# Performance work log

Hardware: AMD Instinct MI355X
Metric: run time of the kernel (lower is better)

The kernel has to match this reference:

```python
import jax, jax.numpy as jnp
import numpy as np

B, S, D = 2, 1024, 768      # batch, seq, d_model
F, F_UP = 8192, 8192        # downstream / upstream dictionary sizes
K = 64                      # top-k of the downstream AE
MASK_DENSITY = 0.05         # fraction of allowed feature-feature connections


def setup_inputs() -> dict:
    key = jax.random.key(0)
    ks = jax.random.split(key, 12)
    inv_sqrt_d = 1.0 / np.sqrt(D)
    resid = jax.random.normal(ks[0], (B, S, D), dtype=jnp.float32)
    # upstream pruned features: k-sparse-ish non-negative activations
    pruned0 = jax.nn.relu(jax.random.normal(ks[1], (B, S, F_UP)) - 2.0).astype(jnp.float32)
    pruned1 = jax.nn.relu(jax.random.normal(ks[2], (B, S, F_UP)) - 2.0).astype(jnp.float32)
    feature_buffer = jnp.zeros((B, S, F), dtype=jnp.float32)
    W_enc = jax.random.normal(ks[3], (F, D), dtype=jnp.float32) * inv_sqrt_d
    b_enc = jax.random.normal(ks[4], (F,), dtype=jnp.float32) * 0.01
    W_dec = jax.random.normal(ks[5], (F, D), dtype=jnp.float32) * inv_sqrt_d
    b_dec = jax.random.normal(ks[6], (D,), dtype=jnp.float32) * 0.01
    W_dec_up0 = jax.random.normal(ks[7], (F_UP, D), dtype=jnp.float32) * inv_sqrt_d
    W_dec_up1 = jax.random.normal(ks[8], (F_UP, D), dtype=jnp.float32) * inv_sqrt_d
    b_dec_up0 = jax.random.normal(ks[9], (D,), dtype=jnp.float32) * 0.01
    b_dec_up1 = jax.random.normal(ks[10], (D,), dtype=jnp.float32) * 0.01
    km0, km1 = jax.random.split(ks[11])
    mask0 = (jax.random.uniform(km0, (F, F_UP)) < MASK_DENSITY).astype(jnp.float32)
    mask1 = (jax.random.uniform(km1, (F, F_UP)) < MASK_DENSITY).astype(jnp.float32)
    return {
        "resid": resid, "pruned0": pruned0, "pruned1": pruned1,
        "feature_buffer": feature_buffer,
        "W_enc": W_enc, "b_enc": b_enc, "W_dec": W_dec, "b_dec": b_dec,
        "W_dec_up0": W_dec_up0, "W_dec_up1": W_dec_up1,
        "b_dec_up0": b_dec_up0, "b_dec_up1": b_dec_up1,
        "mask0": mask0, "mask1": mask1, "k": K,
    }


def reference(resid, pruned0, pruned1, feature_buffer,
              W_enc, b_enc, W_dec, b_dec,
              W_dec_up0, W_dec_up1, b_dec_up0, b_dec_up1,
              mask0, mask1, k):
    # initial contributions: encode the cached residual stream, [B,S,F]
    approx = jnp.einsum("bsd,fd->bsf", resid, W_enc)
    upstream_bias = b_dec_up0 + b_dec_up1
    # accumulate connection-masked upstream contributions
    for pruned, W_dec_up, mask in ((pruned0, W_dec_up0, mask0),
                                   (pruned1, W_dec_up1, mask1)):
        # masked virtual weights: [F, F_up]
        virtual = jnp.einsum("fd,ud->fu", W_enc, W_dec_up) * mask
        approx = approx + jnp.einsum("bsu,fu->bsf", pruned, virtual)
    # bias correction: project summed upstream decoder biases, add encoder bias
    approx = approx + jnp.einsum("fd,d->f", W_enc, upstream_bias) + b_enc
    # topk (unsorted set equals torch's sorted=False), relu, scatter into buffer
    top_vals, top_idx = jax.lax.top_k(approx, k)        # [B,S,k]
    top_vals = jax.nn.relu(top_vals)
    Bn, Sn, Fn = feature_buffer.shape
    bi = jnp.arange(Bn)[:, None, None]
    si = jnp.arange(Sn)[None, :, None]
    feat_buffer = jnp.zeros_like(feature_buffer).at[bi, si, top_idx].set(top_vals)
    # dense decode
    reconstructions = jnp.einsum("bsf,fd->bsd", feat_buffer, W_dec) + b_dec
    return feat_buffer, reconstructions
```

## Files before the change

### kernel.cpp

```cpp
#include <hip/hip_runtime.h>
#include <stdint.h>

typedef unsigned long long u64;
typedef unsigned short u16;

#define F_DIM 8192
#define U_DIM 8192
#define D_DIM 768
#define NTOK  2048
#define KSEL  64
#define ROWCAP 544
#define TILE  256
#define NFT   32
#define NUT   32
#define DCH   32
#define ENTCAP 3840
#define NBIN  1024
#define FT    128
#define TT    128
#define NTT   16
#define PCAP  16

__global__ void k_bias(const float* __restrict__ Wenc, const float* __restrict__ benc,
                       const float* __restrict__ b0, const float* __restrict__ b1,
                       float* __restrict__ t_bias) {
    int wid = threadIdx.x >> 6, lane = threadIdx.x & 63;
    int f = blockIdx.x * 4 + wid;
    const float* row = Wenc + (size_t)f * D_DIM;
    float s = 0.f;
    for (int j = lane; j < D_DIM; j += 64) s += row[j] * (b0[j] + b1[j]);
    #pragma unroll
    for (int off = 32; off; off >>= 1) s += __shfl_down(s, off, 64);
    if (lane == 0) t_bias[f] = s + benc[f];
}

__global__ void k_mask_scan(const float* __restrict__ mask0, const float* __restrict__ mask1,
                            int* __restrict__ rowcnt_tile, u64* __restrict__ bitmap) {
    __shared__ int rc[TILE][4];
    int ut = blockIdx.x, ft = blockIdx.y, l = blockIdx.z;
    const float* mask = l ? mask1 : mask0;
    int tid = threadIdx.x, lane = tid & 63, wid = tid >> 6;
    int u = ut * TILE + tid;
    int f0 = ft * TILE;
    u64* bm = bitmap + (((size_t)(l * NFT + ft) * NUT + ut) * TILE) * 4;
    for (int fl = 0; fl < TILE; ++fl) {
        float v = mask[(size_t)(f0 + fl) * U_DIM + u];
        u64 bal = __ballot(v != 0.0f);
        if (lane == 0) { bm[(size_t)fl * 4 + wid] = bal; rc[fl][wid] = __popcll(bal); }
    }
    __syncthreads();
    rowcnt_tile[(size_t)(l * NUT + ut) * F_DIM + f0 + tid] =
        rc[tid][0] + rc[tid][1] + rc[tid][2] + rc[tid][3];
}

__global__ void k_row_prefix(const int* __restrict__ rowcnt_tile, int* __restrict__ base_r,
                             int* __restrict__ rowcnt_tot) {
    int idx = blockIdx.x * blockDim.x + threadIdx.x;
    int l = idx >> 13, f = idx & (F_DIM - 1);
    int run = 0;
    for (int ut = 0; ut < NUT; ++ut) {
        int c = rowcnt_tile[(size_t)(l * NUT + ut) * F_DIM + f];
        base_r[(size_t)(l * NUT + ut) * F_DIM + f] = run;
        run += c;
    }
    rowcnt_tot[l * F_DIM + f] = run < ROWCAP ? run : ROWCAP;
}

__global__ __launch_bounds__(256, 2) void k_virt_build(
        const float* __restrict__ Wenc, const float* __restrict__ Wup0,
        const float* __restrict__ Wup1, const u64* __restrict__ bitmap,
        const int* __restrict__ base_r, u16* __restrict__ csr_u, float* __restrict__ csr_v) {
    __shared__ u64 bm[TILE][4];
    __shared__ int cs[TILE];
    __shared__ unsigned char entu[ENTCAP];
    __shared__ float acc[ENTCAP];
    __shared__ float wu_t[DCH][TILE + 1];
    int ut = blockIdx.x, ft = blockIdx.y, l = blockIdx.z;
    const float* Wup = l ? Wup1 : Wup0;
    int tid = threadIdx.x;
    int u0 = ut * TILE, f0 = ft * TILE;

    const u64* gbm = bitmap + (((size_t)(l * NFT + ft) * NUT + ut) * TILE) * 4;
    for (int i = tid; i < TILE * 4; i += 256) ((u64*)bm)[i] = gbm[i];
    __syncthreads();

    int cnt = 0;
    #pragma unroll
    for (int w = 0; w < 4; ++w) cnt += (int)__popcll(bm[tid][w]);
    cs[tid] = cnt;
    __syncthreads();
    for (int off = 1; off < 256; off <<= 1) {
        int v = (tid >= off) ? cs[tid - off] : 0;
        __syncthreads();
        cs[tid] += v;
        __syncthreads();
    }
    int cstart = cs[tid] - cnt;
    {
        int i = 0;
        #pragma unroll
        for (int w = 0; w < 4; ++w) {
            u64 word = bm[tid][w];
            while (word) {
                int b = __builtin_ctzll(word); word &= word - 1;
                int p = cstart + i;
                if (p < ENTCAP) entu[p] = (unsigned char)(w * 64 + b);
                ++i;
            }
        }
    }
    for (int i = tid; i < ENTCAP; i += 256) acc[i] = 0.f;
    __syncthreads();

    float we[DCH];
    for (int d0 = 0; d0 < D_DIM; d0 += DCH) {
        const float* ur = Wup + (size_t)(u0 + tid) * D_DIM + d0;
        #pragma unroll
        for (int j = 0; j < DCH; j += 4) {
            float4 t4 = *(const float4*)(ur + j);
            wu_t[j][tid] = t4.x; wu_t[j + 1][tid] = t4.y;
            wu_t[j + 2][tid] = t4.z; wu_t[j + 3][tid] = t4.w;
        }
        const float* wr = Wenc + (size_t)(f0 + tid) * D_DIM + d0;
        #pragma unroll
        for (int j = 0; j < DCH; j += 4) {
            float4 t4 = *(const float4*)(wr + j);
            we[j] = t4.x; we[j + 1] = t4.y; we[j + 2] = t4.z; we[j + 3] = t4.w;
        }
        __syncthreads();
        for (int i = 0; i < cnt; ++i) {
            int p = cstart + i;
            if (p >= ENTCAP) break;
            int ul = entu[p];
            float s = 0.f;
            #pragma unroll
            for (int j = 0; j < DCH; ++j) s += we[j] * wu_t[j][ul];
            acc[p] += s;
        }
        __syncthreads();
    }
    int f = f0 + tid;
    int bse = base_r[(size_t)(l * NUT + ut) * F_DIM + f];
    size_t rb = ((size_t)l * F_DIM + f) * ROWCAP;
    for (int i = 0; i < cnt; ++i) {
        int p = cstart + i;
        if (p >= ENTCAP) break;
        int slot = bse + i;
        if (slot < ROWCAP) {
            csr_u[rb + slot] = (u16)(u0 + entu[p]);
            csr_v[rb + slot] = acc[p];
        }
    }
}

__global__ void k_zero(int* __restrict__ p, int n) {
    int i = (blockIdx.x * blockDim.x + threadIdx.x) * 4;
    if (i < n) *(int4*)(p + i) = make_int4(0, 0, 0, 0);
}

__global__ __launch_bounds__(256) void k_ptok2(
        const float* __restrict__ pruned0, const float* __restrict__ pruned1,
        int* __restrict__ cnt_g, u64* __restrict__ lists) {
    int t = blockIdx.x, l = blockIdx.y;
    int tt = t >> 7, tl = t & (TT - 1);
    const float* Pr = (l ? pruned1 : pruned0) + (size_t)t * U_DIM;
    int* cg = cnt_g + (size_t)(l * NTT + tt) * U_DIM;
    u64* L = lists + (size_t)(l * NTT + tt) * U_DIM * PCAP;
    int tid = threadIdx.x;
    #pragma unroll
    for (int it = 0; it < U_DIM / 1024; ++it) {
        int u0 = it * 1024 + tid * 4;
        float4 v4 = *(const float4*)(Pr + u0);
        float vv[4] = {v4.x, v4.y, v4.z, v4.w};
        #pragma unroll
        for (int j = 0; j < 4; ++j) {
            float v = vv[j];
            if (v != 0.0f) {
                int u = u0 + j;
                int c = atomicAdd(&cg[u], 1);
                if (c < PCAP)
                    L[(size_t)u * PCAP + c] = ((u64)__float_as_uint(v) << 32) | (unsigned)tl;
            }
        }
    }
}

__global__ __launch_bounds__(512, 2) void k_contrib2(
        const u16* __restrict__ csr_u, const float* __restrict__ csr_v,
        const int* __restrict__ rowcnt_tot, const u64* __restrict__ lists,
        const int* __restrict__ cnt_g, float* __restrict__ C) {
    __shared__ float accum[TT][FT + 1];
    __shared__ unsigned char lc[U_DIM];
    int raw = blockIdx.x;
    int xcd = raw & 7, idx = raw >> 3;
    int ft = (xcd << 3) | (idx & 7);
    int tt = idx >> 3;
    int tid = threadIdx.x, lane = tid & 63, wid = tid >> 6;
    for (int i = tid; i < TT * (FT + 1); i += 512) ((float*)accum)[i] = 0.f;
    for (int l = 0; l < 2; ++l) {
        __syncthreads();
        for (int i = tid; i < U_DIM; i += 512) {
            int c = cnt_g[(size_t)(l * NTT + tt) * U_DIM + i];
            lc[i] = (unsigned char)(c < PCAP ? c : PCAP);
        }
        __syncthreads();
        const u64* L = lists + (size_t)(l * NTT + tt) * U_DIM * PCAP;
        for (int r = wid; r < FT; r += 8) {
            int f = ft * FT + r;
            int cnt = rowcnt_tot[l * F_DIM + f];
            size_t rb = ((size_t)l * F_DIM + f) * ROWCAP;
            for (int e = lane; e < cnt; e += 64) {
                int u = csr_u[rb + e];
                float v = csr_v[rb + e];
                int c = lc[u];
                const u64* lp = L + (size_t)u * PCAP;
                for (int j = 0; j < c; ++j) {
                    u64 pk = lp[j];
                    int tok = (int)(unsigned)pk;
                    float p = __uint_as_float((unsigned)(pk >> 32));
                    atomicAdd(&accum[tok][r], p * v);
                }
            }
        }
    }
    __syncthreads();
    int t0 = tt * TT, f0 = ft * FT;
    for (int i = tid; i < TT * FT; i += 512) {
        int tok = i >> 7, r = i & (FT - 1);
        C[(size_t)(t0 + tok) * F_DIM + f0 + r] = accum[tok][r];
    }
}

#define BM 128
#define BN 128
#define BK 16
__global__ __launch_bounds__(256) void k_encoder(
        const float* __restrict__ resid, const float* __restrict__ Wenc,
        const float* __restrict__ t_bias, float* __restrict__ C) {
    __shared__ float As[BK][BM + 4];
    __shared__ float Bs[BK][BN + 4];
    int tid = threadIdx.x;
    int m0 = blockIdx.y * BM, n0 = blockIdx.x * BN;
    int mt = tid & 15, nt = tid >> 4;
    float acc[8][8] = {};
    for (int k0 = 0; k0 < D_DIM; k0 += BK) {
        if (tid < 128) {
            const float* ar = resid + (size_t)(m0 + tid) * D_DIM + k0;
            #pragma unroll
            for (int j = 0; j < BK; j += 4) {
                float4 t4 = *(const float4*)(ar + j);
                As[j][tid] = t4.x; As[j + 1][tid] = t4.y;
                As[j + 2][tid] = t4.z; As[j + 3][tid] = t4.w;
            }
        } else {
            int r = tid - 128;
            const float* br = Wenc + (size_t)(n0 + r) * D_DIM + k0;
            #pragma unroll
            for (int j = 0; j < BK; j += 4) {
                float4 t4 = *(const float4*)(br + j);
                Bs[j][r] = t4.x; Bs[j + 1][r] = t4.y;
                Bs[j + 2][r] = t4.z; Bs[j + 3][r] = t4.w;
            }
        }
        __syncthreads();
        #pragma unroll
        for (int k = 0; k < BK; ++k) {
            float a[8], bb[8];
            *(float4*)&a[0]  = *(const float4*)&As[k][mt * 8];
            *(float4*)&a[4]  = *(const float4*)&As[k][mt * 8 + 4];
            *(float4*)&bb[0] = *(const float4*)&Bs[k][nt * 8];
            *(float4*)&bb[4] = *(const float4*)&Bs[k][nt * 8 + 4];
            #pragma unroll
            for (int i = 0; i < 8; ++i)
                #pragma unroll
                for (int j = 0; j < 8; ++j) acc[i][j] += a[i] * bb[j];
        }
        __syncthreads();
    }
    float tb[8];
    #pragma unroll
    for (int j = 0; j < 8; ++j) tb[j] = t_bias[n0 + nt * 8 + j];
    #pragma unroll
    for (int i = 0; i < 8; ++i) {
        float* cr = C + (size_t)(m0 + mt * 8 + i) * F_DIM + n0 + nt * 8;
        #pragma unroll
        for (int j = 0; j < 8; ++j) cr[j] += acc[i][j] + tb[j];
    }
}

__global__ __launch_bounds__(256) void k_select(
        float* __restrict__ C, int* __restrict__ sel_idx, float* __restrict__ sel_val) {
    __shared__ float row[F_DIM];
    __shared__ int hist[NBIN];
    __shared__ int bstar, nsure, ncand;
    __shared__ float sure_v[64];  __shared__ int sure_f[64];
    __shared__ float cand_v[256]; __shared__ int cand_f[256];
    __shared__ float out_v[KSEL]; __shared__ int out_f[KSEL];
    int t = blockIdx.x, tid = threadIdx.x;
    float* Crow = C + (size_t)t * F_DIM;
    for (int i = tid; i < F_DIM; i += 256) row[i] = Crow[i];
    for (int i = tid; i < NBIN; i += 256) hist[i] = 0;
    __syncthreads();
    for (int i = tid; i < F_DIM; i += 256) {
        int b = (int)floorf((row[i] + 16.0f) * 32.0f);
        b = b < 0 ? 0 : (b > NBIN - 1 ? NBIN - 1 : b);
        atomicAdd(&hist[b], 1);
    }
    __syncthreads();
    if (tid == 0) {
        int cum = 0, bs = 0;
        for (int b = NBIN - 1; b >= 0; --b) { cum += hist[b]; if (cum >= KSEL) { bs = b; break; } }
        bstar = bs; nsure = 0; ncand = 0;
    }
    __syncthreads();
    int bs = bstar;
    for (int i = tid; i < F_DIM; i += 256) {
        float v = row[i];
        int b = (int)floorf((v + 16.0f) * 32.0f);
        b = b < 0 ? 0 : (b > NBIN - 1 ? NBIN - 1 : b);
        if (b > bs) {
            int p = atomicAdd(&nsure, 1);
            if (p < 64) { sure_v[p] = v; sure_f[p] = i; }
        } else if (b == bs) {
            int p = atomicAdd(&ncand, 1);
            if (p < 256) { cand_v[p] = v; cand_f[p] = i; }
        }
    }
    __syncthreads();
    if (tid == 0) {
        int c1 = nsure; if (c1 > KSEL) c1 = KSEL;
        for (int i = 0; i < c1; ++i) { out_v[i] = sure_v[i]; out_f[i] = sure_f[i]; }
        int need = KSEL - c1;
        int nc = ncand; if (nc > 256) nc = 256;
        for (int s = 0; s < need; ++s) {
            float bv = -1e30f; int bf = 0x7fffffff, bi = -1;
            for (int i = 0; i < nc; ++i) {
                float v = cand_v[i];
                if (v > bv || (v == bv && cand_f[i] < bf)) { bv = v; bf = cand_f[i]; bi = i; }
            }
            if (bi < 0) { out_v[c1 + s] = 0.f; out_f[c1 + s] = 0; continue; }
            out_v[c1 + s] = cand_v[bi]; out_f[c1 + s] = cand_f[bi];
            cand_v[bi] = -1e30f;
        }
    }
    __syncthreads();
    for (int i = tid; i < F_DIM; i += 256) Crow[i] = 0.0f;
    __syncthreads();
    if (tid < KSEL) {
        float v = out_v[tid]; int f = out_f[tid];
        float rv = v > 0.f ? v : 0.f;
        Crow[f] = rv;
        sel_idx[t * KSEL + tid] = f;
        sel_val[t * KSEL + tid] = rv;
    }
}

__global__ __launch_bounds__(256) void k_decode(
        const int* __restrict__ sel_idx, const float* __restrict__ sel_val,
        const float* __restrict__ Wdec, const float* __restrict__ bdec,
        float* __restrict__ recon) {
    __shared__ int sf[KSEL]; __shared__ float sv[KSEL];
    int t = blockIdx.x, tid = threadIdx.x;
    if (tid < KSEL) { sf[tid] = sel_idx[t * KSEL + tid]; sv[tid] = sel_val[t * KSEL + tid]; }
    __syncthreads();
    for (int d = tid; d < D_DIM; d += 256) {
        float s = bdec[d];
        #pragma unroll 8
        for (int j = 0; j < KSEL; ++j) s += sv[j] * Wdec[(size_t)sf[j] * D_DIM + d];
        recon[(size_t)t * D_DIM + d] = s;
    }
}

extern "C" void kernel_launch(void* const* d_in, const int* in_sizes, int n_in,
                              void* d_out, int out_size, void* d_ws, size_t ws_size,
                              hipStream_t stream) {
    (void)in_sizes; (void)n_in; (void)out_size; (void)ws_size;
    const float* resid   = (const float*)d_in[0];
    const float* pruned0 = (const float*)d_in[1];
    const float* pruned1 = (const float*)d_in[2];
    const float* Wenc    = (const float*)d_in[4];
    const float* benc    = (const float*)d_in[5];
    const float* Wdec    = (const float*)d_in[6];
    const float* bdec    = (const float*)d_in[7];
    const float* Wup0    = (const float*)d_in[8];
    const float* Wup1    = (const float*)d_in[9];
    const float* bup0    = (const float*)d_in[10];
    const float* bup1    = (const float*)d_in[11];
    const float* mask0   = (const float*)d_in[12];
    const float* mask1   = (const float*)d_in[13];

    char* ws = (char*)d_ws;
    size_t o = 0;
    auto alloc = [&](size_t bytes) -> char* {
        o = (o + 255) & ~(size_t)255;
        char* p = ws + o; o += bytes; return p;
    };
    float* t_bias      = (float*)alloc((size_t)F_DIM * 4);
    int*   rowcnt_tile = (int*)  alloc((size_t)2 * NUT * F_DIM * 4);
    int*   base_r      = (int*)  alloc((size_t)2 * NUT * F_DIM * 4);
    int*   rowcnt_tot  = (int*)  alloc((size_t)2 * F_DIM * 4);
    u64*   bitmap      = (u64*)  alloc((size_t)2 * NFT * NUT * TILE * 4 * 8);
    u16*   csr_u       = (u16*)  alloc((size_t)2 * F_DIM * ROWCAP * 2);
    float* csr_v       = (float*)alloc((size_t)2 * F_DIM * ROWCAP * 4);
    u64*   lists       = (u64*)  alloc((size_t)2 * NTT * U_DIM * PCAP * 8);
    int*   cnt_g       = (int*)  alloc((size_t)2 * NTT * U_DIM * 4);
    int*   sel_idx     = (int*)  alloc((size_t)NTOK * KSEL * 4);
    float* sel_val     = (float*)alloc((size_t)NTOK * KSEL * 4);

    float* out   = (float*)d_out;
    float* C     = out;
    float* recon = out + (size_t)NTOK * F_DIM;

    const int NCNT = 2 * NTT * U_DIM;

    hipLaunchKernelGGL(k_bias,       dim3(F_DIM / 4),        dim3(256), 0, stream,
                       Wenc, benc, bup0, bup1, t_bias);
    hipLaunchKernelGGL(k_mask_scan,  dim3(NUT, NFT, 2),      dim3(256), 0, stream,
                       mask0, mask1, rowcnt_tile, bitmap);
    hipLaunchKernelGGL(k_row_prefix, dim3(2 * F_DIM / 256),  dim3(256), 0, stream,
                       rowcnt_tile, base_r, rowcnt_tot);
    hipLaunchKernelGGL(k_zero,       dim3(NCNT / 1024),      dim3(256), 0, stream,
                       cnt_g, NCNT);
    hipLaunchKernelGGL(k_virt_build, dim3(NUT, NFT, 2),      dim3(256), 0, stream,
                       Wenc, Wup0, Wup1, bitmap, base_r, csr_u, csr_v);
    hipLaunchKernelGGL(k_ptok2,      dim3(NTOK, 2),          dim3(256), 0, stream,
                       pruned0, pruned1, cnt_g, lists);
    hipLaunchKernelGGL(k_contrib2,   dim3(8 * 8 * NTT),      dim3(512), 0, stream,
                       csr_u, csr_v, rowcnt_tot, lists, cnt_g, C);
    hipLaunchKernelGGL(k_encoder,    dim3(F_DIM / BN, NTOK / BM), dim3(256), 0, stream,
                       resid, Wenc, t_bias, C);
    hipLaunchKernelGGL(k_select,     dim3(NTOK),             dim3(256), 0, stream,
                       C, sel_idx, sel_val);
    hipLaunchKernelGGL(k_decode,     dim3(NTOK),             dim3(256), 0, stream,
                       sel_idx, sel_val, Wdec, bdec, recon);
}
```

Measured before the change: 4.346 ms.

## Compact per-feature token lists with prefix scan and stage them in LDS chunks

Replaces the fixed-capacity (16 slots) per-upstream-feature token lists with a compacted CSR layout built by a count, scan and fill sequence. The contribution kernel now walks upstream features in chunks of 1024, staging each chunk's packed token entries and offsets in shared memory. It uses the existing per-tile CSR row offsets so each chunk only visits matching mask entries. The feature tile shrinks to 64 with higher occupancy, aiming to cut scattered global reads and padding. The cost is two extra kernel launches and capacity caps (CCAP, LCAP) that could silently truncate entries.

```diff
diff --git a/kernel.cpp b/kernel.cpp
--- a/kernel.cpp
+++ b/kernel.cpp
@@ -2,6 +2,7 @@
 #include <stdint.h>
 
 typedef unsigned long long u64;
+typedef unsigned int u32;
 typedef unsigned short u16;
 
 #define F_DIM 8192
@@ -16,10 +17,14 @@
 #define DCH   32
 #define ENTCAP 3840
 #define NBIN  1024
-#define FT    128
 #define TT    128
 #define NTT   16
-#define PCAP  16
+#define FT3   64
+#define NFB   (F_DIM / FT3)
+#define UCH   1024
+#define NUCH  (U_DIM / UCH)
+#define CCAP  4096
+#define LCAP  32768
 
 __global__ void k_bias(const float* __restrict__ Wenc, const float* __restrict__ benc,
                        const float* __restrict__ b0, const float* __restrict__ b1,
@@ -158,14 +163,13 @@
     if (i < n) *(int4*)(p + i) = make_int4(0, 0, 0, 0);
 }
 
-__global__ __launch_bounds__(256) void k_ptok2(
+__global__ __launch_bounds__(256) void k_ptok_count(
         const float* __restrict__ pruned0, const float* __restrict__ pruned1,
-        int* __restrict__ cnt_g, u64* __restrict__ lists) {
+        int* __restrict__ cnt_g) {
     int t = blockIdx.x, l = blockIdx.y;
-    int tt = t >> 7, tl = t & (TT - 1);
+    int tt = t >> 7;
     const float* Pr = (l ? pruned1 : pruned0) + (size_t)t * U_DIM;
     int* cg = cnt_g + (size_t)(l * NTT + tt) * U_DIM;
-    u64* L = lists + (size_t)(l * NTT + tt) * U_DIM * PCAP;
     int tid = threadIdx.x;
     #pragma unroll
     for (int it = 0; it < U_DIM / 1024; ++it) {
@@ -173,60 +177,130 @@
         float4 v4 = *(const float4*)(Pr + u0);
         float vv[4] = {v4.x, v4.y, v4.z, v4.w};
         #pragma unroll
+        for (int j = 0; j < 4; ++j)
+            if (vv[j] != 0.0f) atomicAdd(&cg[u0 + j], 1);
+    }
+}
+
+__global__ __launch_bounds__(256) void k_ptok_scan(
+        const int* __restrict__ cnt_g, u32* __restrict__ off_u, int* __restrict__ tot_cnt) {
+    __shared__ u32 part[256];
+    int ltt = blockIdx.x;
+    const int* cg = cnt_g + (size_t)ltt * U_DIM;
+    u32* ou = off_u + (size_t)ltt * U_DIM;
+    int tid = threadIdx.x;
+    int b0 = tid * 32;
+    u32 s = 0;
+    for (int j = 0; j < 32; ++j) s += (u32)cg[b0 + j];
+    part[tid] = s;
+    __syncthreads();
+    for (int off = 1; off < 256; off <<= 1) {
+        u32 v = (tid >= off) ? part[tid - off] : 0;
+        __syncthreads();
+        part[tid] += v;
+        __syncthreads();
+    }
+    u32 run = part[tid] - s;
+    for (int j = 0; j < 32; ++j) { ou[b0 + j] = run; run += (u32)cg[b0 + j]; }
+    if (tid == 255) tot_cnt[ltt] = (int)run;
+}
+
+__global__ __launch_bounds__(256) void k_ptok_fill(
+        const float* __restrict__ pruned0, const float* __restrict__ pruned1,
+        int* __restrict__ cnt_g, const u32* __restrict__ off_u,
+        u64* __restrict__ lists_c) {
+    int t = blockIdx.x, l = blockIdx.y;
+    int tt = t >> 7, tl = t & (TT - 1);
+    const float* Pr = (l ? pruned1 : pruned0) + (size_t)t * U_DIM;
+    int ltt = l * NTT + tt;
+    int* cg = cnt_g + (size_t)ltt * U_DIM;
+    const u32* ou = off_u + (size_t)ltt * U_DIM;
+    u64* Lc = lists_c + (size_t)ltt * LCAP;
+    int tid = threadIdx.x;
+    #pragma unroll
+    for (int it = 0; it < U_DIM / 1024; ++it) {
+        int u0 = it * 1024 + tid * 4;
+        float4 v4 = *(const float4*)(Pr + u0);
+        float vv[4] = {v4.x, v4.y, v4.z, v4.w};
+        #pragma unroll
         for (int j = 0; j < 4; ++j) {
             float v = vv[j];
             if (v != 0.0f) {
                 int u = u0 + j;
-                int c = atomicAdd(&cg[u], 1);
-                if (c < PCAP)
-                    L[(size_t)u * PCAP + c] = ((u64)__float_as_uint(v) << 32) | (unsigned)tl;
-            }
-        }
-    }
-}
-
-__global__ __launch_bounds__(512, 2) void k_contrib2(
+                int a = atomicSub(&cg[u], 1) - 1;
+                u32 slot = ou[u] + (u32)a;
+                if (slot < (u32)LCAP)
+                    Lc[slot] = ((u64)__float_as_uint(v) << 32) | (unsigned)tl;
+            }
+        }
+    }
+}
+
+__global__ __launch_bounds__(512, 4) void k_contrib3(
         const u16* __restrict__ csr_u, const float* __restrict__ csr_v,
-        const int* __restrict__ rowcnt_tot, const u64* __restrict__ lists,
-        const int* __restrict__ cnt_g, float* __restrict__ C) {
-    __shared__ float accum[TT][FT + 1];
-    __shared__ unsigned char lc[U_DIM];
+        const int* __restrict__ base_r, const int* __restrict__ rowcnt_tot,
+        const u32* __restrict__ off_u, const int* __restrict__ tot_cnt,
+        const u64* __restrict__ lists_c, float* __restrict__ C) {
+    __shared__ float accum[TT][FT3 + 1];
+    __shared__ u32 soff[UCH + 1];
+    __shared__ u64 cbuf[CCAP];
     int raw = blockIdx.x;
     int xcd = raw & 7, idx = raw >> 3;
-    int ft = (xcd << 3) | (idx & 7);
-    int tt = idx >> 3;
+    int ft = idx & (NFB - 1);
+    int tth = idx >> 7;
+    int tt = xcd + 8 * tth;
     int tid = threadIdx.x, lane = tid & 63, wid = tid >> 6;
-    for (int i = tid; i < TT * (FT + 1); i += 512) ((float*)accum)[i] = 0.f;
+    for (int i = tid; i < TT * (FT3 + 1); i += 512) ((float*)accum)[i] = 0.f;
     for (int l = 0; l < 2; ++l) {
-        __syncthreads();
-        for (int i = tid; i < U_DIM; i += 512) {
-            int c = cnt_g[(size_t)(l * NTT + tt) * U_DIM + i];
-            lc[i] = (unsigned char)(c < PCAP ? c : PCAP);
-        }
-        __syncthreads();
-        const u64* L = lists + (size_t)(l * NTT + tt) * U_DIM * PCAP;
-        for (int r = wid; r < FT; r += 8) {
-            int f = ft * FT + r;
-            int cnt = rowcnt_tot[l * F_DIM + f];
-            size_t rb = ((size_t)l * F_DIM + f) * ROWCAP;
-            for (int e = lane; e < cnt; e += 64) {
-                int u = csr_u[rb + e];
-                float v = csr_v[rb + e];
-                int c = lc[u];
-                const u64* lp = L + (size_t)u * PCAP;
-                for (int j = 0; j < c; ++j) {
-                    u64 pk = lp[j];
-                    int tok = (int)(unsigned)pk;
-                    float p = __uint_as_float((unsigned)(pk >> 32));
-                    atomicAdd(&accum[tok][r], p * v);
+        int ltt = l * NTT + tt;
+        const u32* offs = off_u + (size_t)ltt * U_DIM;
+        const u64* Lc = lists_c + (size_t)ltt * LCAP;
+        for (int uc = 0; uc < NUCH; ++uc) {
+            __syncthreads();
+            int ub = uc * UCH;
+            for (int i = tid; i < UCH + 1; i += 512) {
+                int u = ub + i;
+                soff[i] = (u < U_DIM) ? offs[u] : (u32)tot_cnt[ltt];
+            }
+            __syncthreads();
+            u32 cbase = soff[0];
+            int scount = (int)(soff[UCH] - cbase);
+            if (scount > CCAP) scount = CCAP;
+            for (int i = tid; i < scount; i += 512) cbuf[i] = Lc[cbase + i];
+            __syncthreads();
+            int ut0 = uc * (UCH / TILE);
+            #pragma unroll
+            for (int rr = 0; rr < FT3 / 8; ++rr) {
+                int r = wid * 8 + rr;
+                int f = ft * FT3 + r;
+                int tot = rowcnt_tot[l * F_DIM + f];
+                int s0 = base_r[(size_t)(l * NUT + ut0) * F_DIM + f];
+                int s1 = (ut0 + 4 < NUT) ? base_r[(size_t)(l * NUT + ut0 + 4) * F_DIM + f]
+                                         : 0x7fffffff;
+                if (s0 > tot) s0 = tot;
+                if (s1 > tot) s1 = tot;
+                size_t rb = ((size_t)l * F_DIM + f) * ROWCAP;
+                for (int e = s0 + lane; e < s1; e += 64) {
+                    int u = csr_u[rb + e];
+                    float v = csr_v[rb + e];
+                    int ul = u - ub;
+                    u32 o0 = soff[ul] - cbase;
+                    u32 o1 = soff[ul + 1] - cbase;
+                    if (o1 > (u32)CCAP) o1 = (u32)CCAP;
+                    for (u32 j = o0; j < o1; ++j) {
+                        u64 pk = cbuf[j];
+                        int tok = (int)(unsigned)pk;
+                        float p = __uint_as_float((unsigned)(pk >> 32));
+                        atomicAdd(&accum[tok][r], p * v);
+                    }
                 }
             }
         }
     }
     __syncthreads();
-    int t0 = tt * TT, f0 = ft * FT;
-    for (int i = tid; i < TT * FT; i += 512) {
-        int tok = i >> 7, r = i & (FT - 1);
+    int t0 = tt * TT, f0 = ft * FT3;
+    for (int i = tid; i < TT * FT3; i += 512) {
+        int tok = i >> 6, r = i & (FT3 - 1);
         C[(size_t)(t0 + tok) * F_DIM + f0 + r] = accum[tok][r];
     }
 }
@@ -402,7 +476,9 @@
     u64*   bitmap      = (u64*)  alloc((size_t)2 * NFT * NUT * TILE * 4 * 8);
     u16*   csr_u       = (u16*)  alloc((size_t)2 * F_DIM * ROWCAP * 2);
     float* csr_v       = (float*)alloc((size_t)2 * F_DIM * ROWCAP * 4);
-    u64*   lists       = (u64*)  alloc((size_t)2 * NTT * U_DIM * PCAP * 8);
+    u32*   off_u       = (u32*)  alloc((size_t)2 * NTT * U_DIM * 4);
+    int*   tot_cnt     = (int*)  alloc((size_t)2 * NTT * 4);
+    u64*   lists_c     = (u64*)  alloc((size_t)2 * NTT * LCAP * 8);
     int*   cnt_g       = (int*)  alloc((size_t)2 * NTT * U_DIM * 4);
     int*   sel_idx     = (int*)  alloc((size_t)NTOK * KSEL * 4);
     float* sel_val     = (float*)alloc((size_t)NTOK * KSEL * 4);
@@ -423,10 +499,14 @@
                        cnt_g, NCNT);
     hipLaunchKernelGGL(k_virt_build, dim3(NUT, NFT, 2),      dim3(256), 0, stream,
                        Wenc, Wup0, Wup1, bitmap, base_r, csr_u, csr_v);
-    hipLaunchKernelGGL(k_ptok2,      dim3(NTOK, 2),          dim3(256), 0, stream,
-                       pruned0, pruned1, cnt_g, lists);
-    hipLaunchKernelGGL(k_contrib2,   dim3(8 * 8 * NTT),      dim3(512), 0, stream,
-                       csr_u, csr_v, rowcnt_tot, lists, cnt_g, C);
+    hipLaunchKernelGGL(k_ptok_count, dim3(NTOK, 2),          dim3(256), 0, stream,
+                       pruned0, pruned1, cnt_g);
+    hipLaunchKernelGGL(k_ptok_scan,  dim3(2 * NTT),          dim3(256), 0, stream,
+                       cnt_g, off_u, tot_cnt);
+    hipLaunchKernelGGL(k_ptok_fill,  dim3(NTOK, 2),          dim3(256), 0, stream,
+                       pruned0, pruned1, cnt_g, off_u, lists_c);
+    hipLaunchKernelGGL(k_contrib3,   dim3(NFB * NTT),        dim3(512), 0, stream,
+                       csr_u, csr_v, base_r, rowcnt_tot, off_u, tot_cnt, lists_c, C);
     hipLaunchKernelGGL(k_encoder,    dim3(F_DIM / BN, NTOK / BM), dim3(256), 0, stream,
                        resid, Wenc, t_bias, C);
     hipLaunchKernelGGL(k_select,     dim3(NTOK),             dim3(256), 0, stream,
```

Result: slower. 4.611 ms (+6.1%).
